# Kernel optimization log

Hardware: AMD Instinct MI355X
Metric: run time of the kernel (lower is better)

## Reference

```python
import jax, jax.numpy as jnp
import numpy as np

B, T, D = 2, 512, 512
E, K = 8, 2
N_CONV, N_MAMBA = 4, 4
KCONV = 7            # conv-expert depthwise kernel
DI = 2 * D           # expert hidden width (expand=2), also Mamba d_inner
DS = 16              # Mamba d_state
DCONV = 4            # Mamba depthwise conv kernel
DTR = 32             # dt_rank = ceil(d_model/16)
WIN = 64             # entropy sliding window


def dw_causal_conv(h, w, b):
    # h: (B,T,C), w: (C,k), b: (C,). Depthwise causal conv (left pad k-1).
    k = w.shape[-1]
    hp = jnp.pad(h, ((0, 0), (k - 1, 0), (0, 0))).transpose(0, 2, 1)  # (B,C,T+k-1)
    out = jax.lax.conv_general_dilated(
        hp, w[:, None, :], (1,), 'VALID',
        dimension_numbers=('NCH', 'OIH', 'NCH'), feature_group_count=h.shape[-1])
    return out.transpose(0, 2, 1) + b


def spectral_entropy(x):
    v = x.mean(-1)                                   # (B,T)
    c1 = jnp.cumsum(v, axis=1)
    c2 = jnp.cumsum(v * v, axis=1)
    sh = lambda c: jnp.pad(c, ((0, 0), (WIN, 0)))[:, :c.shape[1]]
    mu = (c1 - sh(c1)) / WIN
    mu2 = (c2 - sh(c2)) / WIN
    var = jax.nn.relu(mu2 - mu * mu)
    return ((jnp.log(var + 1e-6) + 10.0) / 20.0)[..., None]   # (B,T,1)


def conv_expert(x, fi_w, fi_b, cw, cb, fo_w, fo_b):
    h = jax.nn.gelu(x @ fi_w.T + fi_b)
    h = dw_causal_conv(h, cw, cb)
    return jax.nn.gelu(h) @ fo_w.T + fo_b


def selective_scan(u, delta, A, Bm, Cm, Dm):
    # u, delta: (B,T,DI); A: (DI,DS); Bm, Cm: (B,T,DS); Dm: (DI,)
    dA = jnp.exp(delta[..., None] * A)                          # (B,T,DI,DS)
    dBu = delta[..., None] * Bm[:, :, None, :] * u[..., None]   # (B,T,DI,DS)

    def step(h, inp):
        dA_t, dBu_t, C_t = inp
        h = dA_t * h + dBu_t
        return h, jnp.einsum('bds,bs->bd', h, C_t)

    h0 = jnp.zeros((u.shape[0], A.shape[0], A.shape[1]), u.dtype)
    _, ys = jax.lax.scan(step, h0, (dA.swapaxes(0, 1), dBu.swapaxes(0, 1), Cm.swapaxes(0, 1)))
    return ys.swapaxes(0, 1) + u * Dm


def mamba_expert(x, in_w, cw, cb, xp_w, dt_w, dt_b, Alog, Dm, out_w):
    u, z = jnp.split(x @ in_w.T, 2, axis=-1)            # (B,T,DI) each
    u = jax.nn.silu(dw_causal_conv(u, cw, cb))
    proj = u @ xp_w.T                                    # (B,T,DTR+2*DS)
    dt, Bm, Cm = proj[..., :DTR], proj[..., DTR:DTR + DS], proj[..., DTR + DS:]
    delta = jax.nn.softplus(dt @ dt_w.T + dt_b)
    y = selective_scan(u, delta, -jnp.exp(Alog), Bm, Cm, Dm)
    return (y * jax.nn.silu(z)) @ out_w.T


def setup_inputs() -> dict:
    key = jax.random.key(0)
    ks = iter(jax.random.split(key, 32))
    n = lambda shape, s=0.02: jax.random.normal(next(ks), shape, jnp.float32) * s
    return dict(
        x=jax.random.normal(next(ks), (B, T, D), jnp.float32),
        norm_w=jnp.ones((D,), jnp.float32),
        gate_w=n((E, D)), ent_w=n((E, 1)), ent_b=jnp.zeros((E,), jnp.float32),
        temp=jnp.ones((1,), jnp.float32),
        conv_fc_in_w=n((N_CONV, DI, D)), conv_fc_in_b=jnp.zeros((N_CONV, DI), jnp.float32),
        conv_dw_w=n((N_CONV, DI, KCONV), 0.1), conv_dw_b=jnp.zeros((N_CONV, DI), jnp.float32),
        conv_fc_out_w=n((N_CONV, D, DI)), conv_fc_out_b=jnp.zeros((N_CONV, D), jnp.float32),
        mam_in_w=n((N_MAMBA, 2 * DI, D)),
        mam_conv_w=n((N_MAMBA, DI, DCONV), 0.1), mam_conv_b=jnp.zeros((N_MAMBA, DI), jnp.float32),
        mam_xproj_w=n((N_MAMBA, DTR + 2 * DS, DI)),
        mam_dt_w=n((N_MAMBA, DI, DTR)), mam_dt_b=jnp.full((N_MAMBA, DI), -4.0, jnp.float32),
        mam_Alog=jnp.tile(jnp.log(jnp.arange(1, DS + 1, dtype=jnp.float32)), (N_MAMBA, DI, 1)),
        mam_D=jnp.ones((N_MAMBA, DI), jnp.float32),
        mam_out_w=n((N_MAMBA, D, DI)),
    )


def reference(x, norm_w, gate_w, ent_w, ent_b, temp,
              conv_fc_in_w, conv_fc_in_b, conv_dw_w, conv_dw_b, conv_fc_out_w, conv_fc_out_b,
              mam_in_w, mam_conv_w, mam_conv_b, mam_xproj_w, mam_dt_w, mam_dt_b,
              mam_Alog, mam_D, mam_out_w):
    residual = x
    xn = x * jax.lax.rsqrt(jnp.mean(x * x, -1, keepdims=True) + 1e-6) * norm_w
    ent = spectral_entropy(xn)
    logits = xn @ gate_w.T + ent @ ent_w.T + ent_b
    logits = logits / (jnp.abs(temp) + 1e-6)             # (B,T,E)
    rw, sel = jax.lax.top_k(logits, K)
    rw = jax.nn.softmax(rw, axis=-1)
    # load-balance aux loss on post-temperature logits
    counts = jax.nn.one_hot(sel, E, dtype=jnp.float32).sum(2)
    aux = E * (counts.mean((0, 1)) * jax.nn.softmax(logits, -1).mean((0, 1))).sum()
    # dense expert application, masked-combine (matches torch module)
    out = jnp.zeros_like(xn)
    for e in range(N_CONV):
        wm = jnp.where(sel == e, rw, 0.0).sum(-1)
        y = conv_expert(xn, conv_fc_in_w[e], conv_fc_in_b[e], conv_dw_w[e], conv_dw_b[e],
                        conv_fc_out_w[e], conv_fc_out_b[e])
        out = out + y * wm[..., None]
    for m in range(N_MAMBA):
        e = N_CONV + m
        wm = jnp.where(sel == e, rw, 0.0).sum(-1)
        y = mamba_expert(xn, mam_in_w[m], mam_conv_w[m], mam_conv_b[m], mam_xproj_w[m],
                         mam_dt_w[m], mam_dt_b[m], mam_Alog[m], mam_D[m], mam_out_w[m])
        out = out + y * wm[..., None]
    return out + residual, aux
```

## Files before the change

kernel.cpp:

```cpp
#include <hip/hip_runtime.h>
#include <math.h>

#define B_    2
#define T_    512
#define D_    512
#define E_    8
#define DI_   1024
#define DS_   16
#define DTR_  32
#define WIN_  64
#define BT_   (B_*T_)
#define BTD_  (BT_*D_)
#define NC_   16
#define LCH_  32

typedef unsigned short u16;
typedef __attribute__((ext_vector_type(8))) short bf16x8;
typedef __attribute__((ext_vector_type(4))) float f32x4;

__device__ __forceinline__ float gelu_f(float x) {
    float x3 = x * x * x;
    return 0.5f * x * (1.0f + tanhf(0.7978845608028654f * (x + 0.044715f * x3)));
}
__device__ __forceinline__ float silu_f(float x) {
    return x / (1.0f + __expf(-x));
}
__device__ __forceinline__ float softplus_f(float x) {
    return (x > 20.0f) ? x : log1pf(__expf(x));
}
__device__ __forceinline__ u16 f2bf(float x) {
    union { float f; unsigned u; } v; v.f = x;
    unsigned r = v.u + 0x7fffu + ((v.u >> 16) & 1u);
    return (u16)(r >> 16);
}
__device__ __forceinline__ float bf2f(u16 x) {
    union { unsigned u; float f; } v; v.u = ((unsigned)x) << 16; return v.f;
}
__device__ __forceinline__ void gload_lds16(const u16* g, u16* l) {
    __builtin_amdgcn_global_load_lds((const __attribute__((address_space(1))) void*)g,
                                     (__attribute__((address_space(3))) void*)l, 16, 0, 0);
}

#define DW7T_ 10747904
#define DW4T_ 10776576

__global__ __launch_bounds__(256) void prep_kernel(
    const float* __restrict__ x, const float* __restrict__ nw,
    const float4* __restrict__ cfi, const float4* __restrict__ minw,
    const float4* __restrict__ cfo, const float4* __restrict__ mow4,
    const float4* __restrict__ mxp4, const float* __restrict__ cdw,
    const float* __restrict__ mcw, u16* __restrict__ wpool,
    float* __restrict__ xn, u16* __restrict__ xnb, float* __restrict__ v,
    float* __restrict__ out, float* __restrict__ proj)
{
    const int bid = blockIdx.x, tid = threadIdx.x;
    const int gtid = bid * 256 + tid;

    for (int i = gtid; i < 2686976 + 45056; i += 1024 * 256) {
        if (i < 2686976) {
            float4 val; size_t dg;
            if (i < 524288) {
                int e = i >> 17, r = i & 131071;
                val = cfi[i]; dg = (size_t)e * 393216 + r;
            } else if (i < 1572864) {
                int off = i - 524288;
                int e = off >> 18, r = off & 262143;
                val = minw[off]; dg = (size_t)e * 393216 + 131072 + r;
            } else if (i < 2097152) {
                val = cfo[i - 1572864]; dg = i;
            } else if (i < 2621440) {
                val = mow4[i - 2097152]; dg = i;
            } else {
                val = mxp4[i - 2621440]; dg = i;
            }
            ushort4 o;
            o.x = f2bf(val.x); o.y = f2bf(val.y); o.z = f2bf(val.z); o.w = f2bf(val.w);
            *(ushort4*)(wpool + dg * 4) = o;
        } else {
            int k = i - 2686976;
            if (k < 28672) {
                int z = k / 7168, r = k % 7168;
                int c = r / 7, j = r % 7;
                wpool[DW7T_ + z * 7168 + j * 1024 + c] = f2bf(cdw[k]);
            } else {
                int k2 = k - 28672;
                int z = k2 / 4096, r = k2 % 4096;
                int c = r / 4, j = r % 4;
                wpool[DW4T_ + z * 4096 + j * 1024 + c] = f2bf(mcw[k2]);
            }
        }
    }

    ((float2*)out)[gtid] = ((const float2*)x)[gtid];
    proj[gtid] = 0.f;
    if (gtid == 0) out[BTD_] = 0.f;

    __shared__ float sb[4], sb2[4];
    int t = bid;
    const float* xr = x + (size_t)t * D_;
    float s = 0.f;
    for (int i = tid; i < D_; i += 256) { float a = xr[i]; s += a * a; }
    for (int o = 32; o > 0; o >>= 1) s += __shfl_down(s, o);
    if ((tid & 63) == 0) sb[tid >> 6] = s;
    __syncthreads();
    float tot = sb[0] + sb[1] + sb[2] + sb[3];
    float scale = rsqrtf(tot / (float)D_ + 1e-6f);
    float vs = 0.f;
    for (int i = tid; i < D_; i += 256) {
        float a = xr[i] * scale * nw[i];
        xn[(size_t)t * D_ + i] = a;
        xnb[(size_t)t * D_ + i] = f2bf(a);
        vs += a;
    }
    for (int o = 32; o > 0; o >>= 1) vs += __shfl_down(vs, o);
    if ((tid & 63) == 0) sb2[tid >> 6] = vs;
    __syncthreads();
    if (tid == 0) v[t] = (sb2[0] + sb2[1] + sb2[2] + sb2[3]) / (float)D_;
}

__global__ __launch_bounds__(256) void gating_kernel(
    const float* __restrict__ xn, const float* __restrict__ v,
    const float* __restrict__ gw, const float* __restrict__ ew,
    const float* __restrict__ eb, const float* __restrict__ temp,
    float* __restrict__ wm, float* __restrict__ probs)
{
    int wave = threadIdx.x >> 6, lane = threadIdx.x & 63;
    int t = blockIdx.x * 4 + wave;
    int tloc = t & (T_ - 1);
    int base = t - tloc;
    int j = tloc - (WIN_ - 1) + lane;
    float vv = (j >= 0) ? v[base + j] : 0.f;
    float s1 = vv, s2 = vv * vv;
#pragma unroll
    for (int o = 32; o > 0; o >>= 1) { s1 += __shfl_down(s1, o); s2 += __shfl_down(s2, o); }
    const float* xr = xn + (size_t)t * D_;
    float l[E_];
#pragma unroll
    for (int e = 0; e < E_; ++e) {
        float s = 0.f;
        for (int i = lane; i < D_; i += 64) s += xr[i] * gw[e * D_ + i];
#pragma unroll
        for (int o = 32; o > 0; o >>= 1) s += __shfl_down(s, o);
        l[e] = s;
    }
    if (lane == 0) {
        float mu  = s1 / (float)WIN_;
        float mu2 = s2 / (float)WIN_;
        float var = fmaxf(mu2 - mu * mu, 0.f);
        float ev  = (logf(var + 1e-6f) + 10.f) / 20.f;
        float ts = 1.f / (fabsf(temp[0]) + 1e-6f);
#pragma unroll
        for (int e = 0; e < E_; ++e) l[e] = (l[e] + ev * ew[e] + eb[e]) * ts;
        int i1 = 0;
        for (int e = 1; e < E_; ++e) if (l[e] > l[i1]) i1 = e;
        int i2 = -1;
        for (int e = 0; e < E_; ++e) { if (e == i1) continue; if (i2 < 0 || l[e] > l[i2]) i2 = e; }
        float e2 = __expf(l[i2] - l[i1]);
        float Z = 1.f + e2;
#pragma unroll
        for (int e = 0; e < E_; ++e) wm[t * E_ + e] = 0.f;
        wm[t * E_ + i1] = 1.f / Z;
        wm[t * E_ + i2] = e2 / Z;
        float mm = l[0];
        for (int e = 1; e < E_; ++e) mm = fmaxf(mm, l[e]);
        float Zs = 0.f; float p[E_];
#pragma unroll
        for (int e = 0; e < E_; ++e) { p[e] = __expf(l[e] - mm); Zs += p[e]; }
#pragma unroll
        for (int e = 0; e < E_; ++e) probs[t * E_ + e] = p[e] / Zs;
    }
}

__global__ __launch_bounds__(256) void compact_stats_kernel(
    const float* __restrict__ wm, const float* __restrict__ probs,
    int* __restrict__ idxl, int* __restrict__ cnt, float* __restrict__ out_aux)
{
    int e = blockIdx.x;
    int tid = threadIdx.x;
    int wid = tid >> 6, lane = tid & 63;
    __shared__ int wsum[4];
    __shared__ int base;
    __shared__ float psum[4];
    if (tid == 0) base = 0;
    __syncthreads();
    float ps = 0.f;
    for (int chunk = 0; chunk < 4; ++chunk) {
        int t = chunk * 256 + tid;
        bool f = wm[t * E_ + e] > 0.f;
        ps += probs[t * E_ + e];
        unsigned long long m = __ballot(f);
        if (lane == 0) wsum[wid] = __popcll(m);
        __syncthreads();
        int off = base;
        for (int w = 0; w < wid; ++w) off += wsum[w];
        off += __popcll(m & ((1ull << lane) - 1ull));
        if (f) idxl[e * 1024 + off] = t;
        __syncthreads();
        if (tid == 0) base += wsum[0] + wsum[1] + wsum[2] + wsum[3];
        __syncthreads();
    }
#pragma unroll
    for (int o = 32; o > 0; o >>= 1) ps += __shfl_down(ps, o);
    if (lane == 0) psum[wid] = ps;
    __syncthreads();
    if (tid == 0) {
        cnt[e] = base;
        float pt = psum[0] + psum[1] + psum[2] + psum[3];
        atomicAdd(out_aux, (float)E_ * ((float)base / (float)BT_) * (pt / (float)BT_));
    }
}


__global__ __launch_bounds__(256) void fused_in_gemm_kernel(
    const u16* __restrict__ xnb, const u16* __restrict__ wfused,
    const float* __restrict__ cfi_b, u16* __restrict__ hb, u16* __restrict__ uzb)
{
    const int z = blockIdx.z;
    const int nt = blockIdx.x;
    const bool isA = nt < 16;
    const int bn = (isA ? nt : nt - 16) * 64;
    const int bm = blockIdx.y * 64;
    const u16* A = xnb;
    const u16* W = wfused + (size_t)z * 1572864 + (isA ? 0 : 524288);

    __shared__ u16 As[64 * 64];
    __shared__ u16 Bs[64 * 64];
    const int tid  = threadIdx.x;
    const int wave = tid >> 6, lane = tid & 63;
    const int quad = lane >> 4, r16 = lane & 15;
    const int wm_ = (wave >> 1) * 32, wn = (wave & 1) * 32;

    const int s0 = tid, s1 = 256 + tid;
    const int r0 = s0 >> 3, q0 = (s0 & 7) ^ (r0 & 7);
    const int r1 = s1 >> 3, q1 = (s1 & 7) ^ (r1 & 7);
    const u16* Ag0 = A + (size_t)(bm + r0) * 512 + q0 * 8;
    const u16* Ag1 = A + (size_t)(bm + r1) * 512 + q1 * 8;
    const u16* Wg0 = W + (size_t)(bn + r0) * 512 + q0 * 8;
    const u16* Wg1 = W + (size_t)(bn + r1) * 512 + q1 * 8;

    f32x4 acc[2][2];
    const f32x4 zero = {0.f, 0.f, 0.f, 0.f};
    acc[0][0] = zero; acc[0][1] = zero; acc[1][0] = zero; acc[1][1] = zero;

    for (int k0 = 0; k0 < 512; k0 += 64) {
        gload_lds16(Ag0 + k0, As + tid * 8);
        gload_lds16(Ag1 + k0, As + (256 + tid) * 8);
        gload_lds16(Wg0 + k0, Bs + tid * 8);
        gload_lds16(Wg1 + k0, Bs + (256 + tid) * 8);
        __syncthreads();
#pragma unroll
        for (int ks = 0; ks < 2; ++ks) {
            bf16x8 af[2], bfr[2];
#pragma unroll
            for (int mi = 0; mi < 2; ++mi) {
                int row = wm_ + mi * 16 + r16;
                int p = (ks * 4 + quad) ^ (row & 7);
                af[mi] = *(const bf16x8*)(As + row * 64 + p * 8);
            }
#pragma unroll
            for (int ni = 0; ni < 2; ++ni) {
                int row = wn + ni * 16 + r16;
                int p = (ks * 4 + quad) ^ (row & 7);
                bfr[ni] = *(const bf16x8*)(Bs + row * 64 + p * 8);
            }
#pragma unroll
            for (int mi = 0; mi < 2; ++mi)
#pragma unroll
                for (int ni = 0; ni < 2; ++ni)
                    acc[mi][ni] = __builtin_amdgcn_mfma_f32_16x16x32_bf16(
                        af[mi], bfr[ni], acc[mi][ni], 0, 0, 0);
        }
        __syncthreads();
    }

#pragma unroll
    for (int mi = 0; mi < 2; ++mi) {
#pragma unroll
        for (int vv = 0; vv < 4; ++vv) {
            int m = bm + wm_ + mi * 16 + quad * 4 + vv;
#pragma unroll
            for (int ni = 0; ni < 2; ++ni) {
                int n = bn + wn + ni * 16 + r16;
                float val = acc[mi][ni][vv];
                if (isA) {
                    val = gelu_f(val + cfi_b[z * DI_ + n]);
                    hb[(size_t)z * BT_ * DI_ + (size_t)m * DI_ + n] = f2bf(val);
                } else {
                    uzb[(size_t)z * BT_ * 2048 + (size_t)m * 2048 + n] = f2bf(val);
                }
            }
        }
    }
}

__global__ __launch_bounds__(256) void out_gemm_kernel(
    const u16* __restrict__ Ab, const u16* __restrict__ Wb,
    const float* __restrict__ cfo_b, float* __restrict__ out,
    const float* __restrict__ wmv, const int* __restrict__ idxl,
    const int* __restrict__ cnt)
{
    const int z = blockIdx.z;
    const int count = cnt[z];
    const int bm = blockIdx.y * 64;
    if (bm >= count) return;
    const int bn = blockIdx.x * 64;
    const u16* A = Ab + (size_t)z * BT_ * DI_;
    const u16* W = Wb + (size_t)z * 524288;
    const int* il = idxl + z * 1024;

    __shared__ u16 As[64 * 64];
    __shared__ u16 Bs[64 * 64];
    const int tid  = threadIdx.x;
    const int wave = tid >> 6, lane = tid & 63;
    const int quad = lane >> 4, r16 = lane & 15;
    const int wm_ = (wave >> 1) * 32, wn = (wave & 1) * 32;

    const int s0 = tid, s1 = 256 + tid;
    const int r0 = s0 >> 3, q0 = (s0 & 7) ^ (r0 & 7);
    const int r1 = s1 >> 3, q1 = (s1 & 7) ^ (r1 & 7);
    const int tok0 = il[min(bm + r0, count - 1)];
    const int tok1 = il[min(bm + r1, count - 1)];
    const u16* Ag0 = A + (size_t)tok0 * 1024 + q0 * 8;
    const u16* Ag1 = A + (size_t)tok1 * 1024 + q1 * 8;
    const u16* Wg0 = W + (size_t)(bn + r0) * 1024 + q0 * 8;
    const u16* Wg1 = W + (size_t)(bn + r1) * 1024 + q1 * 8;

    f32x4 acc[2][2];
    const f32x4 zero = {0.f, 0.f, 0.f, 0.f};
    acc[0][0] = zero; acc[0][1] = zero; acc[1][0] = zero; acc[1][1] = zero;

    for (int k0 = 0; k0 < 1024; k0 += 64) {
        gload_lds16(Ag0 + k0, As + tid * 8);
        gload_lds16(Ag1 + k0, As + (256 + tid) * 8);
        gload_lds16(Wg0 + k0, Bs + tid * 8);
        gload_lds16(Wg1 + k0, Bs + (256 + tid) * 8);
        __syncthreads();
#pragma unroll
        for (int ks = 0; ks < 2; ++ks) {
            bf16x8 af[2], bfr[2];
#pragma unroll
            for (int mi = 0; mi < 2; ++mi) {
                int row = wm_ + mi * 16 + r16;
                int p = (ks * 4 + quad) ^ (row & 7);
                af[mi] = *(const bf16x8*)(As + row * 64 + p * 8);
            }
#pragma unroll
            for (int ni = 0; ni < 2; ++ni) {
                int row = wn + ni * 16 + r16;
                int p = (ks * 4 + quad) ^ (row & 7);
                bfr[ni] = *(const bf16x8*)(Bs + row * 64 + p * 8);
            }
#pragma unroll
            for (int mi = 0; mi < 2; ++mi)
#pragma unroll
                for (int ni = 0; ni < 2; ++ni)
                    acc[mi][ni] = __builtin_amdgcn_mfma_f32_16x16x32_bf16(
                        af[mi], bfr[ni], acc[mi][ni], 0, 0, 0);
        }
        __syncthreads();
    }

#pragma unroll
    for (int mi = 0; mi < 2; ++mi) {
#pragma unroll
        for (int vv = 0; vv < 4; ++vv) {
            int mrow = bm + wm_ + mi * 16 + quad * 4 + vv;
            if (mrow >= count) continue;
            int tok = il[mrow];
            float wmval = wmv[tok * E_ + z];
#pragma unroll
            for (int ni = 0; ni < 2; ++ni) {
                int n = bn + wn + ni * 16 + r16;
                float val = acc[mi][ni][vv];
                if (z < 4) val += cfo_b[z * D_ + n];
                atomicAdd(&out[(size_t)tok * D_ + n], val * wmval);
            }
        }
    }
}

template<int SPLITK>
__global__ __launch_bounds__(256) void xproj_gemm_kernel(
    const u16* __restrict__ Ab, size_t sAe, int lda,
    const u16* __restrict__ Wb, size_t sWe, int ldw,
    float* __restrict__ Cp, size_t sCe, int ldc, int K)
{
    const int z = blockIdx.z / SPLITK;
    const int ks_ = blockIdx.z % SPLITK;
    const u16* A = Ab + (size_t)z * sAe;
    const u16* W = Wb + (size_t)z * sWe;

    __shared__ u16 As[64 * 64];
    __shared__ u16 Bs[64 * 64];
    const int tid  = threadIdx.x;
    const int wave = tid >> 6;
    const int lane = tid & 63;
    const int quad = lane >> 4;
    const int r16  = lane & 15;
    const int bm = blockIdx.y * 64;
    const int bn = blockIdx.x * 64;
    const int wm_ = (wave >> 1) * 32;
    const int wn = (wave & 1) * 32;

    const int s0 = tid, s1 = 256 + tid;
    const int r0 = s0 >> 3, q0 = (s0 & 7) ^ (r0 & 7);
    const int r1 = s1 >> 3, q1 = (s1 & 7) ^ (r1 & 7);
    const u16* Ag0 = A + (size_t)(bm + r0) * lda + q0 * 8;
    const u16* Ag1 = A + (size_t)(bm + r1) * lda + q1 * 8;
    const u16* Wg0 = W + (size_t)(bn + r0) * ldw + q0 * 8;
    const u16* Wg1 = W + (size_t)(bn + r1) * ldw + q1 * 8;

    f32x4 acc[2][2];
    const f32x4 zero = {0.f, 0.f, 0.f, 0.f};
    acc[0][0] = zero; acc[0][1] = zero; acc[1][0] = zero; acc[1][1] = zero;

    const int kBeg = ks_ * (K / SPLITK);
    const int kEnd = kBeg + K / SPLITK;
    for (int k0 = kBeg; k0 < kEnd; k0 += 64) {
        gload_lds16(Ag0 + k0, As + tid * 8);
        gload_lds16(Ag1 + k0, As + (256 + tid) * 8);
        gload_lds16(Wg0 + k0, Bs + tid * 8);
        gload_lds16(Wg1 + k0, Bs + (256 + tid) * 8);
        __syncthreads();
#pragma unroll
        for (int kss = 0; kss < 2; ++kss) {
            bf16x8 af[2], bfr[2];
#pragma unroll
            for (int mi = 0; mi < 2; ++mi) {
                int row = wm_ + mi * 16 + r16;
                int p = (kss * 4 + quad) ^ (row & 7);
                af[mi] = *(const bf16x8*)(As + row * 64 + p * 8);
            }
#pragma unroll
            for (int ni = 0; ni < 2; ++ni) {
                int row = wn + ni * 16 + r16;
                int p = (kss * 4 + quad) ^ (row & 7);
                bfr[ni] = *(const bf16x8*)(Bs + row * 64 + p * 8);
            }
#pragma unroll
            for (int mi = 0; mi < 2; ++mi)
#pragma unroll
                for (int ni = 0; ni < 2; ++ni)
                    acc[mi][ni] = __builtin_amdgcn_mfma_f32_16x16x32_bf16(
                        af[mi], bfr[ni], acc[mi][ni], 0, 0, 0);
        }
        __syncthreads();
    }

#pragma unroll
    for (int mi = 0; mi < 2; ++mi) {
#pragma unroll
        for (int vv = 0; vv < 4; ++vv) {
            int m = bm + wm_ + mi * 16 + quad * 4 + vv;
#pragma unroll
            for (int ni = 0; ni < 2; ++ni) {
                int n = bn + wn + ni * 16 + r16;
                atomicAdd(&(Cp + (size_t)z * sCe)[(size_t)m * ldc + n], acc[mi][ni][vv]);
            }
        }
    }
}

__global__ __launch_bounds__(256) void dt_gemm_kernel(
    const float* __restrict__ proj, const float* __restrict__ dtw,
    const float* __restrict__ dtb, float* __restrict__ delta)
{
    const int z = blockIdx.z;
    const float* A = proj + (size_t)z * BT_ * 64;
    const float* W = dtw + (size_t)z * DI_ * DTR_;
    const float* bias = dtb + (size_t)z * DI_;
    float* C = delta + (size_t)z * BT_ * DI_;

    __shared__ float As[16][68];
    __shared__ float Ws[16][68];
    const int bm = blockIdx.y * 64, bn = blockIdx.x * 64;
    const int tid = threadIdx.x;
    const int tx = tid & 15, ty = tid >> 4;
    const int lm = tid >> 2, lk = (tid & 3) * 4;

    const float* Ap = A + (size_t)(bm + lm) * 64 + lk;
    const float* Wp = W + (size_t)(bn + lm) * DTR_ + lk;

    float acc[4][4] = {};
    for (int k0 = 0; k0 < DTR_; k0 += 16) {
        float4 av = *(const float4*)(Ap + k0);
        float4 wv = *(const float4*)(Wp + k0);
        __syncthreads();
        As[lk + 0][lm] = av.x; As[lk + 1][lm] = av.y;
        As[lk + 2][lm] = av.z; As[lk + 3][lm] = av.w;
        Ws[lk + 0][lm] = wv.x; Ws[lk + 1][lm] = wv.y;
        Ws[lk + 2][lm] = wv.z; Ws[lk + 3][lm] = wv.w;
        __syncthreads();
#pragma unroll
        for (int k = 0; k < 16; ++k) {
            float4 a = *(const float4*)&As[k][ty * 4];
            float4 w = *(const float4*)&Ws[k][tx * 4];
            acc[0][0] += a.x * w.x; acc[0][1] += a.x * w.y; acc[0][2] += a.x * w.z; acc[0][3] += a.x * w.w;
            acc[1][0] += a.y * w.x; acc[1][1] += a.y * w.y; acc[1][2] += a.y * w.z; acc[1][3] += a.y * w.w;
            acc[2][0] += a.z * w.x; acc[2][1] += a.z * w.y; acc[2][2] += a.z * w.z; acc[2][3] += a.z * w.w;
            acc[3][0] += a.w * w.x; acc[3][1] += a.w * w.y; acc[3][2] += a.w * w.z; acc[3][3] += a.w * w.w;
        }
    }
#pragma unroll
    for (int i = 0; i < 4; ++i) {
        int m = bm + ty * 4 + i;
#pragma unroll
        for (int j = 0; j < 4; ++j) {
            int n = bn + tx * 4 + j;
            C[(size_t)m * DI_ + n] = softplus_f(acc[i][j] + bias[n]);
        }
    }
}

__global__ __launch_bounds__(256) void dwconv_fused_kernel(
    const u16* __restrict__ hb, const u16* __restrict__ w7t, const float* __restrict__ cb,
    u16* __restrict__ gb,
    const u16* __restrict__ uzb, const u16* __restrict__ w4t, const float* __restrict__ mb,
    u16* __restrict__ ucb)
{
    int idx = blockIdx.x * 256 + threadIdx.x;
    if (idx < 4 * BT_ * 128) {
        int z = idx >> 17;
        int r = idx & 131071;
        int c8 = (r & 127) * 8;
        int bt = r >> 7;
        int t = bt & (T_ - 1);
        const u16* hp = hb + (size_t)z * BT_ * DI_ + (size_t)bt * DI_ + c8;
        const u16* wp = w7t + z * 7168 + c8;
        const float* bp = cb + z * DI_ + c8;
        float acc[8];
        float4 b0 = *(const float4*)bp;
        float4 b1 = *(const float4*)(bp + 4);
        acc[0] = b0.x; acc[1] = b0.y; acc[2] = b0.z; acc[3] = b0.w;
        acc[4] = b1.x; acc[5] = b1.y; acc[6] = b1.z; acc[7] = b1.w;
#pragma unroll
        for (int j = 0; j < 7; ++j) {
            int tt = t - 6 + j;
            if (tt >= 0) {
                bf16x8 hv = *(const bf16x8*)(hp + (j - 6) * DI_);
                bf16x8 wv = *(const bf16x8*)(wp + j * 1024);
#pragma unroll
                for (int k = 0; k < 8; ++k)
                    acc[k] += bf2f((u16)hv[k]) * bf2f((u16)wv[k]);
            }
        }
        u16 o[8];
#pragma unroll
        for (int k = 0; k < 8; ++k) o[k] = f2bf(gelu_f(acc[k]));
        *(bf16x8*)(gb + (size_t)z * BT_ * DI_ + (size_t)bt * DI_ + c8) = *(bf16x8*)o;
    } else {
        int i2 = idx - 4 * BT_ * 128;
        int z = i2 >> 17;
        int r = i2 & 131071;
        int c8 = (r & 127) * 8;
        int bt = r >> 7;
        int t = bt & (T_ - 1);
        const u16* up = uzb + (size_t)z * BT_ * 2048 + (size_t)bt * 2048 + c8;
        const u16* wp = w4t + z * 4096 + c8;
        const float* bp = mb + z * DI_ + c8;
        float acc[8];
        float4 b0 = *(const float4*)bp;
        float4 b1 = *(const float4*)(bp + 4);
        acc[0] = b0.x; acc[1] = b0.y; acc[2] = b0.z; acc[3] = b0.w;
        acc[4] = b1.x; acc[5] = b1.y; acc[6] = b1.z; acc[7] = b1.w;
#pragma unroll
        for (int j = 0; j < 4; ++j) {
            int tt = t - 3 + j;
            if (tt >= 0) {
                bf16x8 uv = *(const bf16x8*)(up + (j - 3) * 2048);
                bf16x8 wv = *(const bf16x8*)(wp + j * 1024);
#pragma unroll
                for (int k = 0; k < 8; ++k)
                    acc[k] += bf2f((u16)uv[k]) * bf2f((u16)wv[k]);
            }
        }
        u16 o[8];
#pragma unroll
        for (int k = 0; k < 8; ++k) o[k] = f2bf(silu_f(acc[k]));
        *(bf16x8*)(ucb + (size_t)z * BT_ * DI_ + (size_t)bt * DI_ + c8) = *(bf16x8*)o;
    }
}

__global__ __launch_bounds__(256) void scan1_kernel(
    const float* __restrict__ delta, const u16* __restrict__ uc,
    const float* __restrict__ proj, const float* __restrict__ Alog,
    float2* __restrict__ PH)
{
    int z = blockIdx.y;
    int idx = blockIdx.x * 256 + threadIdx.x;
    int sq = idx & 3;
    int d = (idx >> 2) & (DI_ - 1);
    int c = (idx >> 12) & (NC_ - 1);
    int b = idx >> 16;
    float A[4];
    *(float4*)A = *(const float4*)(Alog + (size_t)z * DI_ * DS_ + d * DS_ + sq * 4);
#pragma unroll
    for (int s = 0; s < 4; ++s) A[s] = -__expf(A[s]);
    int t0 = c * LCH_;
    const float* dp = delta + (size_t)z * BT_ * DI_ + ((size_t)b * T_ + t0) * DI_ + d;
    const u16*   up = uc    + (size_t)z * BT_ * DI_ + ((size_t)b * T_ + t0) * DI_ + d;
    const float* pp = proj  + (size_t)z * BT_ * 64 + ((size_t)b * T_ + t0) * 64 + 32 + sq * 4;
    float h[4] = {}, P[4] = {1.f, 1.f, 1.f, 1.f};
#pragma unroll 4
    for (int t = 0; t < LCH_; ++t) {
        float del = dp[(size_t)t * DI_];
        float uv  = bf2f(up[(size_t)t * DI_]);
        float du  = del * uv;
        float Bv[4];
        *(float4*)Bv = *(const float4*)(pp + t * 64);
#pragma unroll
        for (int s = 0; s < 4; ++s) {
            float dA = __expf(del * A[s]);
            h[s] = dA * h[s] + du * Bv[s];
            P[s] *= dA;
        }
    }
    float2* o = PH + (size_t)z * (B_ * NC_ * DI_ * 16)
              + (size_t)(b * NC_ + c) * (DI_ * 16) + (size_t)d * 16 + sq * 4;
    float4 o0 = {P[0], h[0], P[1], h[1]};
    float4 o1 = {P[2], h[2], P[3], h[3]};
    *(float4*)&o[0] = o0;
    *(float4*)&o[2] = o1;
}

__global__ __launch_bounds__(256) void scan_mid_kernel(
    const float2* __restrict__ PH, float* __restrict__ H)
{
    int gid = blockIdx.x * 256 + threadIdx.x;
    int z = gid >> 15;
    int r = gid & 32767;
    int b = r >> 14;
    int ds16 = r & 16383;
    float h = 0.f;
    for (int c = 0; c < NC_; ++c) {
        size_t idx = (size_t)z * (B_ * NC_ * DI_ * 16) + ((size_t)(b * NC_ + c)) * (DI_ * 16) + ds16;
        H[idx] = h;
        float2 ph = PH[idx];
        h = ph.y + ph.x * h;
    }
}

__global__ __launch_bounds__(256) void scan2_kernel(
    const float* __restrict__ delta, const u16* __restrict__ uc,
    const float* __restrict__ proj, const float* __restrict__ Alog,
    const float* __restrict__ Dm, const float* __restrict__ H,
    const u16* __restrict__ uz, u16* __restrict__ yb)
{
    int z = blockIdx.y;
    int idx = blockIdx.x * 256 + threadIdx.x;
    int sq = idx & 3;
    int d = (idx >> 2) & (DI_ - 1);
    int c = (idx >> 12) & (NC_ - 1);
    int b = idx >> 16;
    float A[4];
    *(float4*)A = *(const float4*)(Alog + (size_t)z * DI_ * DS_ + d * DS_ + sq * 4);
#pragma unroll
    for (int s = 0; s < 4; ++s) A[s] = -__expf(A[s]);
    float Dd = Dm[(size_t)z * DI_ + d];
    float h[4];
    *(float4*)h = *(const float4*)(H + (size_t)z * (B_ * NC_ * DI_ * 16)
        + (size_t)(b * NC_ + c) * (DI_ * 16) + (size_t)d * 16 + sq * 4);
    int t0 = c * LCH_;
    const float* dp = delta + (size_t)z * BT_ * DI_ + ((size_t)b * T_ + t0) * DI_ + d;
    const u16*   up = uc    + (size_t)z * BT_ * DI_ + ((size_t)b * T_ + t0) * DI_ + d;
    const float* pp = proj  + (size_t)z * BT_ * 64 + ((size_t)b * T_ + t0) * 64 + 32 + sq * 4;
    const u16*   zp = uz    + (size_t)z * BT_ * 2048 + ((size_t)b * T_ + t0) * 2048 + DI_ + d;
    u16* yp = yb + (size_t)z * BT_ * DI_ + ((size_t)b * T_ + t0) * DI_ + d;
#pragma unroll 4
    for (int t = 0; t < LCH_; ++t) {
        float del = dp[(size_t)t * DI_];
        float uv  = bf2f(up[(size_t)t * DI_]);
        float du  = del * uv;
        float Bv[4], Cv[4];
        *(float4*)Bv = *(const float4*)(pp + t * 64);
        *(float4*)Cv = *(const float4*)(pp + t * 64 + 16);
        float y = 0.f;
#pragma unroll
        for (int s = 0; s < 4; ++s) {
            float dA = __expf(del * A[s]);
            h[s] = dA * h[s] + du * Bv[s];
            y += h[s] * Cv[s];
        }
        y += __shfl_down(y, 1, 4);
        y += __shfl_down(y, 2, 4);
        if (sq == 0) {
            y += uv * Dd;
            float zval = bf2f(zp[(size_t)t * 2048]);
            yp[(size_t)t * DI_] = f2bf(y * silu_f(zval));
        }
    }
}

extern "C" void kernel_launch(void* const* d_in, const int* in_sizes, int n_in,
                              void* d_out, int out_size, void* d_ws, size_t ws_size,
                              hipStream_t stream)
{
    const float* x      = (const float*)d_in[0];
    const float* norm_w = (const float*)d_in[1];
    const float* gate_w = (const float*)d_in[2];
    const float* ent_w  = (const float*)d_in[3];
    const float* ent_b  = (const float*)d_in[4];
    const float* temp   = (const float*)d_in[5];
    const float* cfi_w  = (const float*)d_in[6];
    const float* cfi_b  = (const float*)d_in[7];
    const float* cdw_w  = (const float*)d_in[8];
    const float* cdw_b  = (const float*)d_in[9];
    const float* cfo_w  = (const float*)d_in[10];
    const float* cfo_b  = (const float*)d_in[11];
    const float* min_w  = (const float*)d_in[12];
    const float* mcw    = (const float*)d_in[13];
    const float* mcb    = (const float*)d_in[14];
    const float* mxp    = (const float*)d_in[15];
    const float* mdtw   = (const float*)d_in[16];
    const float* mdtb   = (const float*)d_in[17];
    const float* mAlog  = (const float*)d_in[18];
    const float* mD     = (const float*)d_in[19];
    const float* mow    = (const float*)d_in[20];

    float* out = (float*)d_out;

    char* wp = (char*)d_ws;
    auto alloc = [&](size_t bytes) { char* r = wp; wp += (bytes + 255) & ~(size_t)255; return r; };

    float* xn    = (float*)alloc((size_t)BTD_ * 4);
    u16*   xnb   = (u16*)  alloc((size_t)BTD_ * 2);
    float* v     = (float*)alloc(BT_ * 4);
    float* wm    = (float*)alloc(BT_ * E_ * 4);
    float* probs = (float*)alloc(BT_ * E_ * 4);
    int*   idxl  = (int*)  alloc(E_ * 1024 * 4);
    int*   cnt   = (int*)  alloc(E_ * 4);
    u16*   wpool = (u16*)  alloc((size_t)10792960 * 2);
    u16* wfused  = wpool;
    u16* wout    = wpool + 6291456;
    u16* mxp_b16 = wpool + 10485760;
    u16* dw7t    = wpool + DW7T_;
    u16* dw4t    = wpool + DW4T_;

    char* pool = alloc((size_t)81 * 1024 * 1024);
    u16*    hb   = (u16*)pool;
    u16*    gb   = (u16*)(pool + (size_t)8 * 1024 * 1024);
    u16*    yb   = (u16*)(pool + (size_t)16 * 1024 * 1024);
    u16*    uzb  = (u16*)(pool + (size_t)24 * 1024 * 1024);
    u16*    ucb  = (u16*)(pool + (size_t)40 * 1024 * 1024);
    float*  proj = (float*)(pool + (size_t)48 * 1024 * 1024);
    float*  delta= (float*)(pool + (size_t)49 * 1024 * 1024);
    float2* sPH  = (float2*)(pool + (size_t)65 * 1024 * 1024);
    float*  sH   = (float*)hb;

    prep_kernel<<<BT_, 256, 0, stream>>>(
        x, norm_w, (const float4*)cfi_w, (const float4*)min_w, (const float4*)cfo_w,
        (const float4*)mow, (const float4*)mxp, cdw_w, mcw, wpool,
        xn, xnb, v, out, proj);

    gating_kernel<<<BT_ / 4, 256, 0, stream>>>(xn, v, gate_w, ent_w, ent_b, temp, wm, probs);
    compact_stats_kernel<<<E_, 256, 0, stream>>>(wm, probs, idxl, cnt, out + BTD_);

    fused_in_gemm_kernel<<<dim3(48, 16, 4), 256, 0, stream>>>(
        xnb, wfused, cfi_b, hb, uzb);

    dwconv_fused_kernel<<<2 * 4 * BT_ * 128 / 256, 256, 0, stream>>>(
        hb, dw7t, cdw_b, gb, uzb, dw4t, mcb, ucb);

    xproj_gemm_kernel<4><<<dim3(1, BT_ / 64, 16), 256, 0, stream>>>(
        ucb, (size_t)BT_ * DI_, DI_, mxp_b16, (size_t)64 * DI_, DI_,
        proj, (size_t)BT_ * 64, 64, DI_);
    dt_gemm_kernel<<<dim3(DI_ / 64, BT_ / 64, 4), 256, 0, stream>>>(
        proj, mdtw, mdtb, delta);

    const int NSC = B_ * NC_ * DI_ * 4 / 256;
    scan1_kernel<<<dim3(NSC, 4), 256, 0, stream>>>(delta, ucb, proj, mAlog, sPH);
    scan_mid_kernel<<<4 * B_ * DI_ * 16 / 256, 256, 0, stream>>>(sPH, sH);
    scan2_kernel<<<dim3(NSC, 4), 256, 0, stream>>>(
        delta, ucb, proj, mAlog, mD, sH, uzb, yb);

    out_gemm_kernel<<<dim3(D_ / 64, BT_ / 64, 8), 256, 0, stream>>>(
        gb, wout, cfo_b, out, wm, idxl, cnt);
}
```

Measured before the change: 312.6 us.

## Fuse dt projection into scan kernels and fold routing compaction into gating

The standalone dt_gemm kernel is removed. Each scan kernel now loads the proj tile and dt weights into shared memory and recomputes softplus(delta) for its 32-step by 64-channel chunk, so the fp32 delta buffer is never written to or read from global memory. The compact_stats kernel is also removed: gating appends token indices per expert with atomic counters, and the aux-loss reduction moves into block 0 of the dwconv kernel. This saves two launches and a large intermediate, but delta is now computed twice (once in each scan pass) and the per-expert token order becomes nondeterministic.

```diff
diff --git a/kernel.cpp b/kernel.cpp
--- a/kernel.cpp
+++ b/kernel.cpp
@@ -51,7 +51,7 @@
     const float4* __restrict__ mxp4, const float* __restrict__ cdw,
     const float* __restrict__ mcw, u16* __restrict__ wpool,
     float* __restrict__ xn, u16* __restrict__ xnb, float* __restrict__ v,
-    float* __restrict__ out, float* __restrict__ proj)
+    float* __restrict__ out, float* __restrict__ proj, int* __restrict__ cnt)
 {
     const int bid = blockIdx.x, tid = threadIdx.x;
     const int gtid = bid * 256 + tid;
@@ -94,6 +94,7 @@
     ((float2*)out)[gtid] = ((const float2*)x)[gtid];
     proj[gtid] = 0.f;
     if (gtid == 0) out[BTD_] = 0.f;
+    if (gtid < E_) cnt[gtid] = 0;
 
     __shared__ float sb[4], sb2[4];
     int t = bid;
@@ -122,7 +123,8 @@
     const float* __restrict__ xn, const float* __restrict__ v,
     const float* __restrict__ gw, const float* __restrict__ ew,
     const float* __restrict__ eb, const float* __restrict__ temp,
-    float* __restrict__ wm, float* __restrict__ probs)
+    float* __restrict__ wm, float* __restrict__ probs,
+    int* __restrict__ idxl, int* __restrict__ cnt)
 {
     int wave = threadIdx.x >> 6, lane = threadIdx.x & 63;
     int t = blockIdx.x * 4 + wave;
@@ -161,6 +163,10 @@
         for (int e = 0; e < E_; ++e) wm[t * E_ + e] = 0.f;
         wm[t * E_ + i1] = 1.f / Z;
         wm[t * E_ + i2] = e2 / Z;
+        int p1 = atomicAdd(&cnt[i1], 1);
+        idxl[i1 * 1024 + p1] = t;
+        int p2 = atomicAdd(&cnt[i2], 1);
+        idxl[i2 * 1024 + p2] = t;
         float mm = l[0];
         for (int e = 1; e < E_; ++e) mm = fmaxf(mm, l[e]);
         float Zs = 0.f; float p[E_];
@@ -168,45 +174,6 @@
         for (int e = 0; e < E_; ++e) { p[e] = __expf(l[e] - mm); Zs += p[e]; }
 #pragma unroll
         for (int e = 0; e < E_; ++e) probs[t * E_ + e] = p[e] / Zs;
-    }
-}
-
-__global__ __launch_bounds__(256) void compact_stats_kernel(
-    const float* __restrict__ wm, const float* __restrict__ probs,
-    int* __restrict__ idxl, int* __restrict__ cnt, float* __restrict__ out_aux)
-{
-    int e = blockIdx.x;
-    int tid = threadIdx.x;
-    int wid = tid >> 6, lane = tid & 63;
-    __shared__ int wsum[4];
-    __shared__ int base;
-    __shared__ float psum[4];
-    if (tid == 0) base = 0;
-    __syncthreads();
-    float ps = 0.f;
-    for (int chunk = 0; chunk < 4; ++chunk) {
-        int t = chunk * 256 + tid;
-        bool f = wm[t * E_ + e] > 0.f;
-        ps += probs[t * E_ + e];
-        unsigned long long m = __ballot(f);
-        if (lane == 0) wsum[wid] = __popcll(m);
-        __syncthreads();
-        int off = base;
-        for (int w = 0; w < wid; ++w) off += wsum[w];
-        off += __popcll(m & ((1ull << lane) - 1ull));
-        if (f) idxl[e * 1024 + off] = t;
-        __syncthreads();
-        if (tid == 0) base += wsum[0] + wsum[1] + wsum[2] + wsum[3];
-        __syncthreads();
-    }
-#pragma unroll
-    for (int o = 32; o > 0; o >>= 1) ps += __shfl_down(ps, o);
-    if (lane == 0) psum[wid] = ps;
-    __syncthreads();
-    if (tid == 0) {
-        cnt[e] = base;
-        float pt = psum[0] + psum[1] + psum[2] + psum[3];
-        atomicAdd(out_aux, (float)E_ * ((float)base / (float)BT_) * (pt / (float)BT_));
     }
 }
 
@@ -461,62 +428,13 @@
     }
 }
 
-__global__ __launch_bounds__(256) void dt_gemm_kernel(
-    const float* __restrict__ proj, const float* __restrict__ dtw,
-    const float* __restrict__ dtb, float* __restrict__ delta)
-{
-    const int z = blockIdx.z;
-    const float* A = proj + (size_t)z * BT_ * 64;
-    const float* W = dtw + (size_t)z * DI_ * DTR_;
-    const float* bias = dtb + (size_t)z * DI_;
-    float* C = delta + (size_t)z * BT_ * DI_;
-
-    __shared__ float As[16][68];
-    __shared__ float Ws[16][68];
-    const int bm = blockIdx.y * 64, bn = blockIdx.x * 64;
-    const int tid = threadIdx.x;
-    const int tx = tid & 15, ty = tid >> 4;
-    const int lm = tid >> 2, lk = (tid & 3) * 4;
-
-    const float* Ap = A + (size_t)(bm + lm) * 64 + lk;
-    const float* Wp = W + (size_t)(bn + lm) * DTR_ + lk;
-
-    float acc[4][4] = {};
-    for (int k0 = 0; k0 < DTR_; k0 += 16) {
-        float4 av = *(const float4*)(Ap + k0);
-        float4 wv = *(const float4*)(Wp + k0);
-        __syncthreads();
-        As[lk + 0][lm] = av.x; As[lk + 1][lm] = av.y;
-        As[lk + 2][lm] = av.z; As[lk + 3][lm] = av.w;
-        Ws[lk + 0][lm] = wv.x; Ws[lk + 1][lm] = wv.y;
-        Ws[lk + 2][lm] = wv.z; Ws[lk + 3][lm] = wv.w;
-        __syncthreads();
-#pragma unroll
-        for (int k = 0; k < 16; ++k) {
-            float4 a = *(const float4*)&As[k][ty * 4];
-            float4 w = *(const float4*)&Ws[k][tx * 4];
-            acc[0][0] += a.x * w.x; acc[0][1] += a.x * w.y; acc[0][2] += a.x * w.z; acc[0][3] += a.x * w.w;
-            acc[1][0] += a.y * w.x; acc[1][1] += a.y * w.y; acc[1][2] += a.y * w.z; acc[1][3] += a.y * w.w;
-            acc[2][0] += a.z * w.x; acc[2][1] += a.z * w.y; acc[2][2] += a.z * w.z; acc[2][3] += a.z * w.w;
-            acc[3][0] += a.w * w.x; acc[3][1] += a.w * w.y; acc[3][2] += a.w * w.z; acc[3][3] += a.w * w.w;
-        }
-    }
-#pragma unroll
-    for (int i = 0; i < 4; ++i) {
-        int m = bm + ty * 4 + i;
-#pragma unroll
-        for (int j = 0; j < 4; ++j) {
-            int n = bn + tx * 4 + j;
-            C[(size_t)m * DI_ + n] = softplus_f(acc[i][j] + bias[n]);
-        }
-    }
-}
-
 __global__ __launch_bounds__(256) void dwconv_fused_kernel(
     const u16* __restrict__ hb, const u16* __restrict__ w7t, const float* __restrict__ cb,
     u16* __restrict__ gb,
     const u16* __restrict__ uzb, const u16* __restrict__ w4t, const float* __restrict__ mb,
-    u16* __restrict__ ucb)
+    u16* __restrict__ ucb,
+    const float* __restrict__ probs, const int* __restrict__ cnt,
+    float* __restrict__ out_aux)
 {
     int idx = blockIdx.x * 256 + threadIdx.x;
     if (idx < 4 * BT_ * 128) {
@@ -579,35 +497,74 @@
         for (int k = 0; k < 8; ++k) o[k] = f2bf(silu_f(acc[k]));
         *(bf16x8*)(ucb + (size_t)z * BT_ * DI_ + (size_t)bt * DI_ + c8) = *(bf16x8*)o;
     }
+
+    if (blockIdx.x == 0) {
+        __shared__ float ps[E_];
+        int tid = threadIdx.x;
+        if (tid < E_) ps[tid] = 0.f;
+        __syncthreads();
+        float loc[E_] = {};
+        for (int t = tid; t < BT_; t += 256)
+#pragma unroll
+            for (int e = 0; e < E_; ++e) loc[e] += probs[t * E_ + e];
+#pragma unroll
+        for (int e = 0; e < E_; ++e) atomicAdd(&ps[e], loc[e]);
+        __syncthreads();
+        if (tid == 0) {
+            float s = 0.f;
+            for (int e = 0; e < E_; ++e)
+                s += ((float)cnt[e] / (float)BT_) * (ps[e] / (float)BT_);
+            out_aux[0] = (float)E_ * s;
+        }
+    }
 }
 
 __global__ __launch_bounds__(256) void scan1_kernel(
-    const float* __restrict__ delta, const u16* __restrict__ uc,
-    const float* __restrict__ proj, const float* __restrict__ Alog,
-    float2* __restrict__ PH)
-{
-    int z = blockIdx.y;
-    int idx = blockIdx.x * 256 + threadIdx.x;
-    int sq = idx & 3;
-    int d = (idx >> 2) & (DI_ - 1);
-    int c = (idx >> 12) & (NC_ - 1);
-    int b = idx >> 16;
+    const u16* __restrict__ uc, const float* __restrict__ proj,
+    const float* __restrict__ Alog, const float* __restrict__ dtw,
+    const float* __restrict__ dtb, float2* __restrict__ PH)
+{
+    const int z = blockIdx.y;
+    const int tid = threadIdx.x;
+    const int d0 = (blockIdx.x * 64) & (DI_ - 1);
+    const int c  = (blockIdx.x >> 4) & (NC_ - 1);
+    const int b  = blockIdx.x >> 8;
+    const int t0 = c * LCH_;
+
+    __shared__ float projs[32][68];
+    __shared__ float dtws[64][33];
+    __shared__ float dls[32][65];
+
+    const float* pbase = proj + (size_t)z * BT_ * 64 + ((size_t)b * T_ + t0) * 64;
+    for (int i = tid; i < 2048; i += 256) projs[i >> 6][i & 63] = pbase[i];
+    const float* wbase = dtw + (size_t)z * DI_ * DTR_ + (size_t)d0 * DTR_;
+    for (int i = tid; i < 2048; i += 256) dtws[i >> 5][i & 31] = wbase[i];
+    __syncthreads();
+    for (int j = tid; j < 2048; j += 256) {
+        int t = j >> 6, dl = j & 63;
+        float acc = dtb[(size_t)z * DI_ + d0 + dl];
+#pragma unroll
+        for (int k = 0; k < DTR_; ++k) acc += projs[t][k] * dtws[dl][k];
+        dls[t][dl] = softplus_f(acc);
+    }
+    __syncthreads();
+
+    const int sq = tid & 3;
+    const int dl = (tid >> 2) & 63;
+    const int d = d0 + dl;
     float A[4];
     *(float4*)A = *(const float4*)(Alog + (size_t)z * DI_ * DS_ + d * DS_ + sq * 4);
 #pragma unroll
     for (int s = 0; s < 4; ++s) A[s] = -__expf(A[s]);
-    int t0 = c * LCH_;
-    const float* dp = delta + (size_t)z * BT_ * DI_ + ((size_t)b * T_ + t0) * DI_ + d;
-    const u16*   up = uc    + (size_t)z * BT_ * DI_ + ((size_t)b * T_ + t0) * DI_ + d;
-    const float* pp = proj  + (size_t)z * BT_ * 64 + ((size_t)b * T_ + t0) * 64 + 32 + sq * 4;
+    const u16* up = uc + (size_t)z * BT_ * DI_ + ((size_t)b * T_ + t0) * DI_ + d;
     float h[4] = {}, P[4] = {1.f, 1.f, 1.f, 1.f};
 #pragma unroll 4
     for (int t = 0; t < LCH_; ++t) {
-        float del = dp[(size_t)t * DI_];
+        float del = dls[t][dl];
         float uv  = bf2f(up[(size_t)t * DI_]);
         float du  = del * uv;
         float Bv[4];
-        *(float4*)Bv = *(const float4*)(pp + t * 64);
+        *(float4*)Bv = *(const float4*)&projs[t][32 + sq * 4];
 #pragma unroll
         for (int s = 0; s < 4; ++s) {
             float dA = __expf(del * A[s]);
@@ -641,17 +598,40 @@
 }
 
 __global__ __launch_bounds__(256) void scan2_kernel(
-    const float* __restrict__ delta, const u16* __restrict__ uc,
-    const float* __restrict__ proj, const float* __restrict__ Alog,
-    const float* __restrict__ Dm, const float* __restrict__ H,
-    const u16* __restrict__ uz, u16* __restrict__ yb)
-{
-    int z = blockIdx.y;
-    int idx = blockIdx.x * 256 + threadIdx.x;
-    int sq = idx & 3;
-    int d = (idx >> 2) & (DI_ - 1);
-    int c = (idx >> 12) & (NC_ - 1);
-    int b = idx >> 16;
+    const u16* __restrict__ uc, const float* __restrict__ proj,
+    const float* __restrict__ Alog, const float* __restrict__ dtw,
+    const float* __restrict__ dtb, const float* __restrict__ Dm,
+    const float* __restrict__ H, const u16* __restrict__ uz,
+    u16* __restrict__ yb)
+{
+    const int z = blockIdx.y;
+    const int tid = threadIdx.x;
+    const int d0 = (blockIdx.x * 64) & (DI_ - 1);
+    const int c  = (blockIdx.x >> 4) & (NC_ - 1);
+    const int b  = blockIdx.x >> 8;
+    const int t0 = c * LCH_;
+
+    __shared__ float projs[32][68];
+    __shared__ float dtws[64][33];
+    __shared__ float dls[32][65];
+
+    const float* pbase = proj + (size_t)z * BT_ * 64 + ((size_t)b * T_ + t0) * 64;
+    for (int i = tid; i < 2048; i += 256) projs[i >> 6][i & 63] = pbase[i];
+    const float* wbase = dtw + (size_t)z * DI_ * DTR_ + (size_t)d0 * DTR_;
+    for (int i = tid; i < 2048; i += 256) dtws[i >> 5][i & 31] = wbase[i];
+    __syncthreads();
+    for (int j = tid; j < 2048; j += 256) {
+        int t = j >> 6, dl = j & 63;
+        float acc = dtb[(size_t)z * DI_ + d0 + dl];
+#pragma unroll
+        for (int k = 0; k < DTR_; ++k) acc += projs[t][k] * dtws[dl][k];
+        dls[t][dl] = softplus_f(acc);
+    }
+    __syncthreads();
+
+    const int sq = tid & 3;
+    const int dl = (tid >> 2) & 63;
+    const int d = d0 + dl;
     float A[4];
     *(float4*)A = *(const float4*)(Alog + (size_t)z * DI_ * DS_ + d * DS_ + sq * 4);
 #pragma unroll
@@ -660,20 +640,17 @@
     float h[4];
     *(float4*)h = *(const float4*)(H + (size_t)z * (B_ * NC_ * DI_ * 16)
         + (size_t)(b * NC_ + c) * (DI_ * 16) + (size_t)d * 16 + sq * 4);
-    int t0 = c * LCH_;
-    const float* dp = delta + (size_t)z * BT_ * DI_ + ((size_t)b * T_ + t0) * DI_ + d;
-    const u16*   up = uc    + (size_t)z * BT_ * DI_ + ((size_t)b * T_ + t0) * DI_ + d;
-    const float* pp = proj  + (size_t)z * BT_ * 64 + ((size_t)b * T_ + t0) * 64 + 32 + sq * 4;
-    const u16*   zp = uz    + (size_t)z * BT_ * 2048 + ((size_t)b * T_ + t0) * 2048 + DI_ + d;
+    const u16* up = uc + (size_t)z * BT_ * DI_ + ((size_t)b * T_ + t0) * DI_ + d;
+    const u16* zp = uz + (size_t)z * BT_ * 2048 + ((size_t)b * T_ + t0) * 2048 + DI_ + d;
     u16* yp = yb + (size_t)z * BT_ * DI_ + ((size_t)b * T_ + t0) * DI_ + d;
 #pragma unroll 4
     for (int t = 0; t < LCH_; ++t) {
-        float del = dp[(size_t)t * DI_];
+        float del = dls[t][dl];
         float uv  = bf2f(up[(size_t)t * DI_]);
         float du  = del * uv;
         float Bv[4], Cv[4];
-        *(float4*)Bv = *(const float4*)(pp + t * 64);
-        *(float4*)Cv = *(const float4*)(pp + t * 64 + 16);
+        *(float4*)Bv = *(const float4*)&projs[t][32 + sq * 4];
+        *(float4*)Cv = *(const float4*)&projs[t][48 + sq * 4];
         float y = 0.f;
 #pragma unroll
         for (int s = 0; s < 4; ++s) {
@@ -736,42 +713,40 @@
     u16* dw7t    = wpool + DW7T_;
     u16* dw4t    = wpool + DW4T_;
 
-    char* pool = alloc((size_t)81 * 1024 * 1024);
+    char* pool = alloc((size_t)65 * 1024 * 1024);
     u16*    hb   = (u16*)pool;
     u16*    gb   = (u16*)(pool + (size_t)8 * 1024 * 1024);
     u16*    yb   = (u16*)(pool + (size_t)16 * 1024 * 1024);
     u16*    uzb  = (u16*)(pool + (size_t)24 * 1024 * 1024);
     u16*    ucb  = (u16*)(pool + (size_t)40 * 1024 * 1024);
     float*  proj = (float*)(pool + (size_t)48 * 1024 * 1024);
-    float*  delta= (float*)(pool + (size_t)49 * 1024 * 1024);
-    float2* sPH  = (float2*)(pool + (size_t)65 * 1024 * 1024);
+    float2* sPH  = (float2*)(pool + (size_t)49 * 1024 * 1024);
     float*  sH   = (float*)hb;
 
     prep_kernel<<<BT_, 256, 0, stream>>>(
         x, norm_w, (const float4*)cfi_w, (const float4*)min_w, (const float4*)cfo_w,
         (const float4*)mow, (const float4*)mxp, cdw_w, mcw, wpool,
-        xn, xnb, v, out, proj);
-
-    gating_kernel<<<BT_ / 4, 256, 0, stream>>>(xn, v, gate_w, ent_w, ent_b, temp, wm, probs);
-    compact_stats_kernel<<<E_, 256, 0, stream>>>(wm, probs, idxl, cnt, out + BTD_);
+        xn, xnb, v, out, proj, cnt);
+
+    gating_kernel<<<BT_ / 4, 256, 0, stream>>>(
+        xn, v, gate_w, ent_w, ent_b, temp, wm, probs, idxl, cnt);
 
     fused_in_gemm_kernel<<<dim3(48, 16, 4), 256, 0, stream>>>(
         xnb, wfused, cfi_b, hb, uzb);
 
     dwconv_fused_kernel<<<2 * 4 * BT_ * 128 / 256, 256, 0, stream>>>(
-        hb, dw7t, cdw_b, gb, uzb, dw4t, mcb, ucb);
+        hb, dw7t, cdw_b, gb, uzb, dw4t, mcb, ucb, probs, cnt, out + BTD_);
 
     xproj_gemm_kernel<4><<<dim3(1, BT_ / 64, 16), 256, 0, stream>>>(
         ucb, (size_t)BT_ * DI_, DI_, mxp_b16, (size_t)64 * DI_, DI_,
         proj, (size_t)BT_ * 64, 64, DI_);
-    dt_gemm_kernel<<<dim3(DI_ / 64, BT_ / 64, 4), 256, 0, stream>>>(
-        proj, mdtw, mdtb, delta);
 
     const int NSC = B_ * NC_ * DI_ * 4 / 256;
-    scan1_kernel<<<dim3(NSC, 4), 256, 0, stream>>>(delta, ucb, proj, mAlog, sPH);
+    scan1_kernel<<<dim3(NSC, 4), 256, 0, stream>>>(
+        ucb, proj, mAlog, mdtw, mdtb, sPH);
     scan_mid_kernel<<<4 * B_ * DI_ * 16 / 256, 256, 0, stream>>>(sPH, sH);
     scan2_kernel<<<dim3(NSC, 4), 256, 0, stream>>>(
-        delta, ucb, proj, mAlog, mD, sH, uzb, yb);
+        ucb, proj, mAlog, mdtw, mdtb, mD, sH, uzb, yb);
 
     out_gemm_kernel<<<dim3(D_ / 64, BT_ / 64, 8), 256, 0, stream>>>(
         gb, wout, cfo_b, out, wm, idxl, cnt);
```

Measured after the change: 359.4 us. 15.0% more time.
